# Kernel optimization log

Hardware: AMD Instinct MI355X
Metric: run time of the kernel (lower is better)

Reference implementation:

```python
import jax, jax.numpy as jnp
import numpy as np

USER_NUM = 100000
ITEM_NUM = 100000
DIM = 64
BS = 256


def setup_inputs() -> dict:
    key = jax.random.key(0)
    k1, k2, k3, k4, k5 = jax.random.split(key, 5)
    # xavier_normal-ish scale for embeddings/linear
    user_table = jax.random.normal(k1, (USER_NUM, DIM), dtype=jnp.float32) * 0.1
    item_table = jax.random.normal(k2, (ITEM_NUM, DIM), dtype=jnp.float32) * 0.1
    cls_w = jax.random.normal(k3, (5, DIM), dtype=jnp.float32) * (2.0 / (DIM + 5)) ** 0.5
    cls_b = jnp.zeros((5,), dtype=jnp.float32)
    batch_user = jax.random.randint(k4, (BS,), 0, USER_NUM, dtype=jnp.int64)
    values = jnp.array([[1.0, 2.0, 3.0, 4.0, 5.0]], dtype=jnp.float32)
    return {
        "batch_user": batch_user,
        "user_table": user_table,
        "item_table": item_table,
        "cls_w": cls_w,
        "cls_b": cls_b,
        "values": values,
    }


def reference(batch_user, user_table, item_table, cls_w, cls_b, values):
    # forward_full_items: score every (user, item) pair.
    # Torch materializes h_ui = (u repeated) * (items tiled) of shape
    # [bs*item_num, dim]; mathematically logits = einsum over dim, so we
    # fuse the broadcasted product with the tiny Linear to avoid the
    # huge expanded intermediate while computing identical math.
    u = user_table[batch_user]                       # [bs, dim]
    # logits[b,i,c] = sum_d u[b,d] * item[i,d] * W[c,d] + b[c]
    logits = jnp.einsum('bd,id,cd->bic', u, item_table, cls_w) + cls_b  # [bs, item_num, 5]
    prob = jax.nn.softmax(logits, axis=-1)
    return jnp.sum(prob * values[0], axis=-1)        # [bs, item_num]
```

## Files before the change

### kernel.cpp

```cpp
#include <hip/hip_runtime.h>

#define I_TOTAL 100000
#define DIM 64
#define BS 256

typedef __attribute__((ext_vector_type(8))) short bf16x8;
typedef __attribute__((ext_vector_type(4))) float f32x4;

__device__ inline unsigned short f2bf(float x) {
    union { float f; unsigned u; } v; v.f = x;
    return (unsigned short)((v.u + 0x8000u) >> 16);
}

__device__ inline unsigned pk_bf16(float lo, float hi) {
    unsigned r;
    asm("v_cvt_pk_bf16_f32 %0, %1, %2" : "=v"(r) : "v"(lo), "v"(hi));
    return r;
}

__device__ inline bf16x8 pack8(float4 a, float4 b) {
    union { unsigned u[4]; bf16x8 v; } r;
    r.u[0] = pk_bf16(a.x, a.y);
    r.u[1] = pk_bf16(a.z, a.w);
    r.u[2] = pk_bf16(b.x, b.y);
    r.u[3] = pk_bf16(b.z, b.w);
    return r.v;
}

__device__ inline float rfl(float x) {
    union { float f; int i; } u; u.f = x;
    u.i = __builtin_amdgcn_readfirstlane(u.i);
    return u.f;
}

__global__ __launch_bounds__(256) void conv_items(
    const float* __restrict__ item, unsigned short* __restrict__ itbf)
{
    long t = (long)blockIdx.x * 256 + threadIdx.x;
    const float4* p = (const float4*)(item + t * 8);
    float4 a = p[0], b = p[1];
    ushort4 r0, r1;
    r0.x = f2bf(a.x); r0.y = f2bf(a.y); r0.z = f2bf(a.z); r0.w = f2bf(a.w);
    r1.x = f2bf(b.x); r1.y = f2bf(b.y); r1.z = f2bf(b.z); r1.w = f2bf(b.w);
    ushort4* q = (ushort4*)(itbf + t * 8);
    q[0] = r0; q[1] = r1;
}

__device__ inline void mfma_tile(const bf16x8 (&afr)[5][2], bf16x8 b0, bf16x8 b1,
                                 f32x4 (&acc)[5])
{
    const f32x4 zero = (f32x4){0.f, 0.f, 0.f, 0.f};
#pragma unroll
    for (int c = 0; c < 5; ++c) {
        acc[c] = __builtin_amdgcn_mfma_f32_16x16x32_bf16(afr[c][0], b0, zero, 0, 0, 0);
        acc[c] = __builtin_amdgcn_mfma_f32_16x16x32_bf16(afr[c][1], b1, acc[c], 0, 0, 0);
    }
}

__device__ inline void softmax_store(const f32x4 (&acc)[5], const float (&sw)[5],
                                     const float (&swv)[5], float* wlds, int ti)
{
#pragma unroll
    for (int rr = 0; rr < 4; ++rr) {
        float e0 = __builtin_amdgcn_exp2f(acc[0][rr]);
        float e1 = __builtin_amdgcn_exp2f(acc[1][rr]);
        float e2 = __builtin_amdgcn_exp2f(acc[2][rr]);
        float e3 = __builtin_amdgcn_exp2f(acc[3][rr]);
        float e4 = __builtin_amdgcn_exp2f(acc[4][rr]);
        float den = e0 * sw[0];
        den = fmaf(e1, sw[1], den);
        den = fmaf(e2, sw[2], den);
        den = fmaf(e3, sw[3], den);
        den = fmaf(e4, sw[4], den);
        float num = e0 * swv[0];
        num = fmaf(e1, swv[1], num);
        num = fmaf(e2, swv[2], num);
        num = fmaf(e3, swv[3], num);
        num = fmaf(e4, swv[4], num);
        wlds[rr * 64 + ti * 16] = num * __builtin_amdgcn_rcpf(den);
    }
}

__global__ __launch_bounds__(64) void gemm_softmax(
    const unsigned short* __restrict__ itbf,
    const int* __restrict__ bu, const float* __restrict__ ut,
    const float* __restrict__ cw, const float* __restrict__ clsb,
    const float* __restrict__ vals, float* __restrict__ out)
{
    __shared__ float ldsb[1056];

    const int blk  = blockIdx.x;
    const int r8   = blk & 7;
    const int rest = blk >> 3;
    const int wv   = rest & 3;
    const int qq   = rest >> 2;
    const int g    = qq & 15;
    const int a    = qq >> 4;
    const int y    = a * 8 + r8;
    if (y >= 98) return;

    const int lane = threadIdx.x & 63;
    const int col  = lane & 15;
    const int quad = lane >> 4;

    const int b_base = g * 16;
    const int i_base = y * 1024 + wv * 256;

    const float s = 1.4426950408889634f;

    const float* up = ut + (size_t)bu[b_base + col] * DIM + quad * 8;
    float4 u0 = *(const float4*)(up);
    float4 u1 = *(const float4*)(up + 4);
    float4 u2 = *(const float4*)(up + 32);
    float4 u3 = *(const float4*)(up + 36);
    u0.x *= s; u0.y *= s; u0.z *= s; u0.w *= s;
    u1.x *= s; u1.y *= s; u1.z *= s; u1.w *= s;
    u2.x *= s; u2.y *= s; u2.z *= s; u2.w *= s;
    u3.x *= s; u3.y *= s; u3.z *= s; u3.w *= s;

    bf16x8 afr[5][2];
    float sw[5], swv[5];
#pragma unroll
    for (int c = 0; c < 5; ++c) {
        const float* wp = cw + c * DIM + quad * 8;
        float4 w0 = *(const float4*)(wp);
        float4 w1 = *(const float4*)(wp + 4);
        float4 w2 = *(const float4*)(wp + 32);
        float4 w3 = *(const float4*)(wp + 36);
        float4 m0 = make_float4(u0.x*w0.x, u0.y*w0.y, u0.z*w0.z, u0.w*w0.w);
        float4 m1 = make_float4(u1.x*w1.x, u1.y*w1.y, u1.z*w1.z, u1.w*w1.w);
        float4 m2 = make_float4(u2.x*w2.x, u2.y*w2.y, u2.z*w2.z, u2.w*w2.w);
        float4 m3 = make_float4(u3.x*w3.x, u3.y*w3.y, u3.z*w3.z, u3.w*w3.w);
        afr[c][0] = pack8(m0, m1);
        afr[c][1] = pack8(m2, m3);
        float w = __builtin_amdgcn_exp2f(clsb[c] * s);
        sw[c]  = rfl(w);
        swv[c] = rfl(w * vals[c]);
    }

    if (y < 97) {
        float* wlds = ldsb + quad * 264 + col;
        const float* rlds = ldsb + quad * 264 + 4 * col;

        float* op[4];
#pragma unroll
        for (int k = 0; k < 4; ++k)
            op[k] = out + (size_t)(b_base + quad * 4 + k) * I_TOTAL + (i_base + 4 * col);

        const unsigned short* bp = itbf + (size_t)(i_base + col) * DIM + quad * 8;

#pragma unroll 1
        for (int t4 = 0; t4 < 4; ++t4) {
#pragma unroll
            for (int ti = 0; ti < 4; ++ti) {
                bf16x8 b0 = *(const bf16x8*)(bp + ti * 1024);
                bf16x8 b1 = *(const bf16x8*)(bp + ti * 1024 + 32);
                f32x4 acc[5];
                mfma_tile(afr, b0, b1, acc);
                softmax_store(acc, sw, swv, wlds, ti);
            }
#pragma unroll
            for (int k = 0; k < 4; ++k) {
                f32x4 o4 = *(const f32x4*)(rlds + k * 64);
                *(f32x4*)op[k] = o4;
                op[k] += 64;
            }
            bp += 4 * 1024;
        }
    } else {
#pragma unroll 1
        for (int t = 0; t < 16; ++t) {
            int i  = i_base + t * 16 + col;
            int ic = i < I_TOTAL ? i : I_TOTAL - 1;
            const unsigned short* p2 = itbf + (size_t)ic * DIM + quad * 8;
            bf16x8 b0 = *(const bf16x8*)p2;
            bf16x8 b1 = *(const bf16x8*)(p2 + 32);
            f32x4 acc[5];
            mfma_tile(afr, b0, b1, acc);
            if (i < I_TOTAL) {
#pragma unroll
                for (int rr = 0; rr < 4; ++rr) {
                    float e0 = __builtin_amdgcn_exp2f(acc[0][rr]);
                    float e1 = __builtin_amdgcn_exp2f(acc[1][rr]);
                    float e2 = __builtin_amdgcn_exp2f(acc[2][rr]);
                    float e3 = __builtin_amdgcn_exp2f(acc[3][rr]);
                    float e4 = __builtin_amdgcn_exp2f(acc[4][rr]);
                    float den = e0 * sw[0];
                    den = fmaf(e1, sw[1], den);
                    den = fmaf(e2, sw[2], den);
                    den = fmaf(e3, sw[3], den);
                    den = fmaf(e4, sw[4], den);
                    float num = e0 * swv[0];
                    num = fmaf(e1, swv[1], num);
                    num = fmaf(e2, swv[2], num);
                    num = fmaf(e3, swv[3], num);
                    num = fmaf(e4, swv[4], num);
                    out[(size_t)(b_base + quad * 4 + rr) * I_TOTAL + i] =
                        num * __builtin_amdgcn_rcpf(den);
                }
            }
        }
    }
}

__global__ __launch_bounds__(256) void gemm_softmax_fb(
    const int* __restrict__ bu, const float* __restrict__ ut,
    const float* __restrict__ it, const float* __restrict__ cw,
    const float* __restrict__ clsb, const float* __restrict__ vals,
    float* __restrict__ out)
{
    __shared__ float ldsb[4224];

    const int blk = blockIdx.x;
    const int r8 = blk & 7;
    const int qq = blk >> 3;
    const int g  = qq & 15;
    const int a  = qq >> 4;
    const int y  = a * 8 + r8;
    if (y >= 98) return;

    const int lane = threadIdx.x & 63;
    const int wave = threadIdx.x >> 6;
    const int col  = lane & 15;
    const int quad = lane >> 4;

    const int b_base = g * 16;
    const int i_base = y * 1024 + wave * 256;

    const float s = 1.4426950408889634f;

    const float* up = ut + (size_t)bu[b_base + col] * DIM + quad * 8;
    float4 u0 = *(const float4*)(up);
    float4 u1 = *(const float4*)(up + 4);
    float4 u2 = *(const float4*)(up + 32);
    float4 u3 = *(const float4*)(up + 36);
    u0.x *= s; u0.y *= s; u0.z *= s; u0.w *= s;
    u1.x *= s; u1.y *= s; u1.z *= s; u1.w *= s;
    u2.x *= s; u2.y *= s; u2.z *= s; u2.w *= s;
    u3.x *= s; u3.y *= s; u3.z *= s; u3.w *= s;

    bf16x8 afr[5][2];
    float sw[5], swv[5];
#pragma unroll
    for (int c = 0; c < 5; ++c) {
        const float* wp = cw + c * DIM + quad * 8;
        float4 w0 = *(const float4*)(wp);
        float4 w1 = *(const float4*)(wp + 4);
        float4 w2 = *(const float4*)(wp + 32);
        float4 w3 = *(const float4*)(wp + 36);
        float4 m0 = make_float4(u0.x*w0.x, u0.y*w0.y, u0.z*w0.z, u0.w*w0.w);
        float4 m1 = make_float4(u1.x*w1.x, u1.y*w1.y, u1.z*w1.z, u1.w*w1.w);
        float4 m2 = make_float4(u2.x*w2.x, u2.y*w2.y, u2.z*w2.z, u2.w*w2.w);
        float4 m3 = make_float4(u3.x*w3.x, u3.y*w3.y, u3.z*w3.z, u3.w*w3.w);
        afr[c][0] = pack8(m0, m1);
        afr[c][1] = pack8(m2, m3);
        float w = __builtin_amdgcn_exp2f(clsb[c] * s);
        sw[c]  = rfl(w);
        swv[c] = rfl(w * vals[c]);
    }

    if (y < 97) {
        float* wlds = ldsb + wave * 1056 + quad * 264 + col;
        const float* rlds = ldsb + wave * 1056 + quad * 264 + 4 * col;

        float* op[4];
#pragma unroll
        for (int k = 0; k < 4; ++k)
            op[k] = out + (size_t)(b_base + quad * 4 + k) * I_TOTAL + (i_base + 4 * col);

        const float* bp = it + (size_t)(i_base + col) * DIM + quad * 8;

#pragma unroll 1
        for (int t4 = 0; t4 < 4; ++t4) {
#pragma unroll
            for (int ti = 0; ti < 4; ++ti) {
                const float* p = bp + ti * 1024;
                float4 q0 = *(const float4*)(p);
                float4 q1 = *(const float4*)(p + 4);
                float4 q2 = *(const float4*)(p + 32);
                float4 q3 = *(const float4*)(p + 36);
                bf16x8 b0 = pack8(q0, q1);
                bf16x8 b1 = pack8(q2, q3);
                f32x4 acc[5];
                mfma_tile(afr, b0, b1, acc);
                softmax_store(acc, sw, swv, wlds, ti);
            }
#pragma unroll
            for (int k = 0; k < 4; ++k) {
                f32x4 o4 = *(const f32x4*)(rlds + k * 64);
                *(f32x4*)op[k] = o4;
                op[k] += 64;
            }
            bp += 4 * 1024;
        }
    } else {
#pragma unroll 1
        for (int t = 0; t < 16; ++t) {
            int i  = i_base + t * 16 + col;
            int ic = i < I_TOTAL ? i : I_TOTAL - 1;
            const float* p2 = it + (size_t)ic * DIM + quad * 8;
            float4 q0 = *(const float4*)(p2);
            float4 q1 = *(const float4*)(p2 + 4);
            float4 q2 = *(const float4*)(p2 + 32);
            float4 q3 = *(const float4*)(p2 + 36);
            bf16x8 b0 = pack8(q0, q1);
            bf16x8 b1 = pack8(q2, q3);
            f32x4 acc[5];
            mfma_tile(afr, b0, b1, acc);
            if (i < I_TOTAL) {
#pragma unroll
                for (int rr = 0; rr < 4; ++rr) {
                    float e0 = __builtin_amdgcn_exp2f(acc[0][rr]);
                    float e1 = __builtin_amdgcn_exp2f(acc[1][rr]);
                    float e2 = __builtin_amdgcn_exp2f(acc[2][rr]);
                    float e3 = __builtin_amdgcn_exp2f(acc[3][rr]);
                    float e4 = __builtin_amdgcn_exp2f(acc[4][rr]);
                    float den = e0 * sw[0];
                    den = fmaf(e1, sw[1], den);
                    den = fmaf(e2, sw[2], den);
                    den = fmaf(e3, sw[3], den);
                    den = fmaf(e4, sw[4], den);
                    float num = e0 * swv[0];
                    num = fmaf(e1, swv[1], num);
                    num = fmaf(e2, swv[2], num);
                    num = fmaf(e3, swv[3], num);
                    num = fmaf(e4, swv[4], num);
                    out[(size_t)(b_base + quad * 4 + rr) * I_TOTAL + i] =
                        num * __builtin_amdgcn_rcpf(den);
                }
            }
        }
    }
}

extern "C" void kernel_launch(void* const* d_in, const int* in_sizes, int n_in,
                              void* d_out, int out_size, void* d_ws, size_t ws_size,
                              hipStream_t stream) {
    const int*   bu   = (const int*)d_in[0];
    const float* ut   = (const float*)d_in[1];
    const float* it   = (const float*)d_in[2];
    const float* cw   = (const float*)d_in[3];
    const float* cb   = (const float*)d_in[4];
    const float* vals = (const float*)d_in[5];
    float* out = (float*)d_out;
    unsigned short* itbf = (unsigned short*)d_ws;

    const size_t needed = (size_t)I_TOTAL * DIM * 2;

    if (ws_size >= needed) {
        conv_items<<<3125, 256, 0, stream>>>(it, itbf);
        gemm_softmax<<<6656, 64, 0, stream>>>(itbf, bu, ut, cw, cb, vals, out);
    } else {
        gemm_softmax_fb<<<1664, 256, 0, stream>>>(bu, ut, it, cw, cb, vals, out);
    }
}
```

Measured before the change: 174.6 us.

## Swap MFMA operands to write output rows directly, dropping LDS transpose

Swapping the MFMA A/B operands transposes the accumulator layout, so each lane holds four consecutive item outputs for one user and can store them as one float4. This removes the LDS staging buffer and its write/read round trip. Full tiles now use nontemporal vector stores and 2x unrolling, and the partial tail is handled per wave. The fallback kernel is restructured the same way into 64-thread blocks. The trade-off is that each wave's stores now spread across 16 user rows, 64 bytes per row, instead of forming longer contiguous segments.

After: 175.1 us. No clear change (+0.3%).

```diff
diff --git a/kernel.cpp b/kernel.cpp
--- a/kernel.cpp
+++ b/kernel.cpp
@@ -46,20 +46,21 @@
     q[0] = r0; q[1] = r1;
 }
 
-__device__ inline void mfma_tile(const bf16x8 (&afr)[5][2], bf16x8 b0, bf16x8 b1,
-                                 f32x4 (&acc)[5])
+__device__ inline void mfma_tile_sw(const bf16x8 (&afr)[5][2], bf16x8 b0, bf16x8 b1,
+                                    f32x4 (&acc)[5])
 {
     const f32x4 zero = (f32x4){0.f, 0.f, 0.f, 0.f};
 #pragma unroll
     for (int c = 0; c < 5; ++c) {
-        acc[c] = __builtin_amdgcn_mfma_f32_16x16x32_bf16(afr[c][0], b0, zero, 0, 0, 0);
-        acc[c] = __builtin_amdgcn_mfma_f32_16x16x32_bf16(afr[c][1], b1, acc[c], 0, 0, 0);
-    }
-}
-
-__device__ inline void softmax_store(const f32x4 (&acc)[5], const float (&sw)[5],
-                                     const float (&swv)[5], float* wlds, int ti)
-{
+        acc[c] = __builtin_amdgcn_mfma_f32_16x16x32_bf16(b0, afr[c][0], zero, 0, 0, 0);
+        acc[c] = __builtin_amdgcn_mfma_f32_16x16x32_bf16(b1, afr[c][1], acc[c], 0, 0, 0);
+    }
+}
+
+__device__ inline f32x4 softmax_vec(const f32x4 (&acc)[5], const float (&sw)[5],
+                                    const float (&swv)[5])
+{
+    f32x4 r;
 #pragma unroll
     for (int rr = 0; rr < 4; ++rr) {
         float e0 = __builtin_amdgcn_exp2f(acc[0][rr]);
@@ -77,8 +78,9 @@
         num = fmaf(e2, swv[2], num);
         num = fmaf(e3, swv[3], num);
         num = fmaf(e4, swv[4], num);
-        wlds[rr * 64 + ti * 16] = num * __builtin_amdgcn_rcpf(den);
-    }
+        r[rr] = num * __builtin_amdgcn_rcpf(den);
+    }
+    return r;
 }
 
 __global__ __launch_bounds__(64) void gemm_softmax(
@@ -87,8 +89,6 @@
     const float* __restrict__ cw, const float* __restrict__ clsb,
     const float* __restrict__ vals, float* __restrict__ out)
 {
-    __shared__ float ldsb[1056];
-
     const int blk  = blockIdx.x;
     const int r8   = blk & 7;
     const int rest = blk >> 3;
@@ -105,6 +105,7 @@
 
     const int b_base = g * 16;
     const int i_base = y * 1024 + wv * 256;
+    if (i_base >= I_TOTAL) return;
 
     const float s = 1.4426950408889634f;
 
@@ -138,94 +139,64 @@
         swv[c] = rfl(w * vals[c]);
     }
 
-    if (y < 97) {
-        float* wlds = ldsb + quad * 264 + col;
-        const float* rlds = ldsb + quad * 264 + 4 * col;
-
-        float* op[4];
-#pragma unroll
-        for (int k = 0; k < 4; ++k)
-            op[k] = out + (size_t)(b_base + quad * 4 + k) * I_TOTAL + (i_base + 4 * col);
-
-        const unsigned short* bp = itbf + (size_t)(i_base + col) * DIM + quad * 8;
-
-#pragma unroll 1
-        for (int t4 = 0; t4 < 4; ++t4) {
-#pragma unroll
-            for (int ti = 0; ti < 4; ++ti) {
-                bf16x8 b0 = *(const bf16x8*)(bp + ti * 1024);
-                bf16x8 b1 = *(const bf16x8*)(bp + ti * 1024 + 32);
-                f32x4 acc[5];
-                mfma_tile(afr, b0, b1, acc);
-                softmax_store(acc, sw, swv, wlds, ti);
-            }
-#pragma unroll
-            for (int k = 0; k < 4; ++k) {
-                f32x4 o4 = *(const f32x4*)(rlds + k * 64);
-                *(f32x4*)op[k] = o4;
-                op[k] += 64;
-            }
-            bp += 4 * 1024;
+    const unsigned short* bp = itbf + (size_t)(i_base + col) * DIM + quad * 8;
+    float* op = out + (size_t)(b_base + col) * I_TOTAL + i_base + quad * 4;
+
+    if (i_base + 256 <= I_TOTAL) {
+#pragma unroll 2
+        for (int t = 0; t < 16; ++t) {
+            bf16x8 b0 = *(const bf16x8*)(bp + t * 1024);
+            bf16x8 b1 = *(const bf16x8*)(bp + t * 1024 + 32);
+            f32x4 acc[5];
+            mfma_tile_sw(afr, b0, b1, acc);
+            f32x4 r = softmax_vec(acc, sw, swv);
+            __builtin_nontemporal_store(r, (f32x4*)(op + t * 16));
         }
     } else {
 #pragma unroll 1
         for (int t = 0; t < 16; ++t) {
-            int i  = i_base + t * 16 + col;
-            int ic = i < I_TOTAL ? i : I_TOTAL - 1;
+            if (i_base + t * 16 >= I_TOTAL) break;
+            int irow = i_base + t * 16 + col;
+            int ic = irow < I_TOTAL ? irow : I_TOTAL - 1;
             const unsigned short* p2 = itbf + (size_t)ic * DIM + quad * 8;
             bf16x8 b0 = *(const bf16x8*)p2;
             bf16x8 b1 = *(const bf16x8*)(p2 + 32);
             f32x4 acc[5];
-            mfma_tile(afr, b0, b1, acc);
-            if (i < I_TOTAL) {
-#pragma unroll
-                for (int rr = 0; rr < 4; ++rr) {
-                    float e0 = __builtin_amdgcn_exp2f(acc[0][rr]);
-                    float e1 = __builtin_amdgcn_exp2f(acc[1][rr]);
-                    float e2 = __builtin_amdgcn_exp2f(acc[2][rr]);
-                    float e3 = __builtin_amdgcn_exp2f(acc[3][rr]);
-                    float e4 = __builtin_amdgcn_exp2f(acc[4][rr]);
-                    float den = e0 * sw[0];
-                    den = fmaf(e1, sw[1], den);
-                    den = fmaf(e2, sw[2], den);
-                    den = fmaf(e3, sw[3], den);
-                    den = fmaf(e4, sw[4], den);
-                    float num = e0 * swv[0];
-                    num = fmaf(e1, swv[1], num);
-                    num = fmaf(e2, swv[2], num);
-                    num = fmaf(e3, swv[3], num);
-                    num = fmaf(e4, swv[4], num);
-                    out[(size_t)(b_base + quad * 4 + rr) * I_TOTAL + i] =
-                        num * __builtin_amdgcn_rcpf(den);
-                }
+            mfma_tile_sw(afr, b0, b1, acc);
+            f32x4 r = softmax_vec(acc, sw, swv);
+            int ie = i_base + t * 16 + quad * 4;
+#pragma unroll
+            for (int rr = 0; rr < 4; ++rr) {
+                if (ie + rr < I_TOTAL)
+                    out[(size_t)(b_base + col) * I_TOTAL + ie + rr] = r[rr];
             }
         }
     }
 }
 
-__global__ __launch_bounds__(256) void gemm_softmax_fb(
+__global__ __launch_bounds__(64) void gemm_softmax_fb(
     const int* __restrict__ bu, const float* __restrict__ ut,
     const float* __restrict__ it, const float* __restrict__ cw,
     const float* __restrict__ clsb, const float* __restrict__ vals,
     float* __restrict__ out)
 {
-    __shared__ float ldsb[4224];
-
-    const int blk = blockIdx.x;
-    const int r8 = blk & 7;
-    const int qq = blk >> 3;
-    const int g  = qq & 15;
-    const int a  = qq >> 4;
-    const int y  = a * 8 + r8;
+    const int blk  = blockIdx.x;
+    const int r8   = blk & 7;
+    const int rest = blk >> 3;
+    const int wv   = rest & 3;
+    const int qq   = rest >> 2;
+    const int g    = qq & 15;
+    const int a    = qq >> 4;
+    const int y    = a * 8 + r8;
     if (y >= 98) return;
 
     const int lane = threadIdx.x & 63;
-    const int wave = threadIdx.x >> 6;
     const int col  = lane & 15;
     const int quad = lane >> 4;
 
     const int b_base = g * 16;
-    const int i_base = y * 1024 + wave * 256;
+    const int i_base = y * 1024 + wv * 256;
+    if (i_base >= I_TOTAL) return;
 
     const float s = 1.4426950408889634f;
 
@@ -259,76 +230,30 @@
         swv[c] = rfl(w * vals[c]);
     }
 
-    if (y < 97) {
-        float* wlds = ldsb + wave * 1056 + quad * 264 + col;
-        const float* rlds = ldsb + wave * 1056 + quad * 264 + 4 * col;
-
-        float* op[4];
-#pragma unroll
-        for (int k = 0; k < 4; ++k)
-            op[k] = out + (size_t)(b_base + quad * 4 + k) * I_TOTAL + (i_base + 4 * col);
-
-        const float* bp = it + (size_t)(i_base + col) * DIM + quad * 8;
-
 #pragma unroll 1
-        for (int t4 = 0; t4 < 4; ++t4) {
-#pragma unroll
-            for (int ti = 0; ti < 4; ++ti) {
-                const float* p = bp + ti * 1024;
-                float4 q0 = *(const float4*)(p);
-                float4 q1 = *(const float4*)(p + 4);
-                float4 q2 = *(const float4*)(p + 32);
-                float4 q3 = *(const float4*)(p + 36);
-                bf16x8 b0 = pack8(q0, q1);
-                bf16x8 b1 = pack8(q2, q3);
-                f32x4 acc[5];
-                mfma_tile(afr, b0, b1, acc);
-                softmax_store(acc, sw, swv, wlds, ti);
-            }
-#pragma unroll
-            for (int k = 0; k < 4; ++k) {
-                f32x4 o4 = *(const f32x4*)(rlds + k * 64);
-                *(f32x4*)op[k] = o4;
-                op[k] += 64;
-            }
-            bp += 4 * 1024;
-        }
-    } else {
-#pragma unroll 1
-        for (int t = 0; t < 16; ++t) {
-            int i  = i_base + t * 16 + col;
-            int ic = i < I_TOTAL ? i : I_TOTAL - 1;
-            const float* p2 = it + (size_t)ic * DIM + quad * 8;
-            float4 q0 = *(const float4*)(p2);
-            float4 q1 = *(const float4*)(p2 + 4);
-            float4 q2 = *(const float4*)(p2 + 32);
-            float4 q3 = *(const float4*)(p2 + 36);
-            bf16x8 b0 = pack8(q0, q1);
-            bf16x8 b1 = pack8(q2, q3);
-            f32x4 acc[5];
-            mfma_tile(afr, b0, b1, acc);
-            if (i < I_TOTAL) {
-#pragma unroll
-                for (int rr = 0; rr < 4; ++rr) {
-                    float e0 = __builtin_amdgcn_exp2f(acc[0][rr]);
-                    float e1 = __builtin_amdgcn_exp2f(acc[1][rr]);
-                    float e2 = __builtin_amdgcn_exp2f(acc[2][rr]);
-                    float e3 = __builtin_amdgcn_exp2f(acc[3][rr]);
-                    float e4 = __builtin_amdgcn_exp2f(acc[4][rr]);
-                    float den = e0 * sw[0];
-                    den = fmaf(e1, sw[1], den);
-                    den = fmaf(e2, sw[2], den);
-                    den = fmaf(e3, sw[3], den);
-                    den = fmaf(e4, sw[4], den);
-                    float num = e0 * swv[0];
-                    num = fmaf(e1, swv[1], num);
-                    num = fmaf(e2, swv[2], num);
-                    num = fmaf(e3, swv[3], num);
-                    num = fmaf(e4, swv[4], num);
-                    out[(size_t)(b_base + quad * 4 + rr) * I_TOTAL + i] =
-                        num * __builtin_amdgcn_rcpf(den);
-                }
-            }
+    for (int t = 0; t < 16; ++t) {
+        if (i_base + t * 16 >= I_TOTAL) break;
+        int irow = i_base + t * 16 + col;
+        int ic = irow < I_TOTAL ? irow : I_TOTAL - 1;
+        const float* p2 = it + (size_t)ic * DIM + quad * 8;
+        float4 q0 = *(const float4*)(p2);
+        float4 q1 = *(const float4*)(p2 + 4);
+        float4 q2 = *(const float4*)(p2 + 32);
+        float4 q3 = *(const float4*)(p2 + 36);
+        bf16x8 b0 = pack8(q0, q1);
+        bf16x8 b1 = pack8(q2, q3);
+        f32x4 acc[5];
+        mfma_tile_sw(afr, b0, b1, acc);
+        f32x4 r = softmax_vec(acc, sw, swv);
+        int ie = i_base + t * 16 + quad * 4;
+        if (ie + 4 <= I_TOTAL) {
+            __builtin_nontemporal_store(r,
+                (f32x4*)(out + (size_t)(b_base + col) * I_TOTAL + ie));
+        } else {
+#pragma unroll
+            for (int rr = 0; rr < 4; ++rr)
+                if (ie + rr < I_TOTAL)
+                    out[(size_t)(b_base + col) * I_TOTAL + ie + rr] = r[rr];
         }
     }
 }
@@ -351,6 +276,6 @@
         conv_items<<<3125, 256, 0, stream>>>(it, itbf);
         gemm_softmax<<<6656, 64, 0, stream>>>(itbf, bu, ut, cw, cb, vals, out);
     } else {
-        gemm_softmax_fb<<<1664, 256, 0, stream>>>(bu, ut, it, cw, cb, vals, out);
-    }
-}
+        gemm_softmax_fb<<<6656, 64, 0, stream>>>(bu, ut, it, cw, cb, vals, out);
+    }
+}
```
